# Optimization experiments

Hardware: AMD Instinct MI355X
Metric: run time of the kernel (lower is better)

## Reference

```python
import jax, jax.numpy as jnp
import numpy as np

B, SE, SD, E, H, V, O = 16, 128, 128, 512, 1024, 32000, 32000


def setup_inputs() -> dict:
    key = jax.random.key(0)
    ks = jax.random.split(key, 14)
    s = 0.02  # small init keeps tanh RNN stable
    return {
        "enc_x": jax.random.randint(ks[0], (B, SE), 0, V),
        "dec_y": jax.random.randint(ks[1], (B, SD), 0, V),
        "state0": jnp.zeros((B, H), jnp.float32),
        "emb": jax.random.normal(ks[2], (V, E), jnp.float32) * s,
        "enc_Wih": jax.random.normal(ks[3], (H, E), jnp.float32) * s,
        "enc_Whh": jax.random.normal(ks[4], (H, H), jnp.float32) * s,
        "enc_b": jax.random.normal(ks[5], (H,), jnp.float32) * s,
        "mlp1_W": jax.random.normal(ks[6], (H, H), jnp.float32) * s,
        "mlp1_b": jax.random.normal(ks[7], (H,), jnp.float32) * s,
        "dec_Wih": jax.random.normal(ks[8], (H, E + H), jnp.float32) * s,
        "dec_Whh": jax.random.normal(ks[9], (H, H), jnp.float32) * s,
        "dec_b": jax.random.normal(ks[10], (H,), jnp.float32) * s,
        "mlp2_W": jax.random.normal(ks[11], (O, H), jnp.float32) * s,
        "mlp2_b": jax.random.normal(ks[12], (O,), jnp.float32) * s,
    }


def _forward(enc_x, dec_y, state0, emb, enc_Wih, enc_Whh, enc_b,
             mlp1_W, mlp1_b, dec_Wih, dec_Whh, dec_b, mlp2_W, mlp2_b):
    # ---- encoder: vanilla tanh RNN over time ----
    enc_emb = emb[enc_x]                      # (B, SE, E)
    xs = jnp.swapaxes(enc_emb, 0, 1)          # (SE, B, E)

    def enc_step(h, x_t):
        h = jnp.tanh(x_t @ enc_Wih.T + h @ enc_Whh.T + enc_b)
        return h, h

    state, hs = jax.lax.scan(enc_step, state0, xs)
    enc_hidden = jnp.swapaxes(hs, 0, 1)       # (B, SE, H)

    # ---- decoder: per-step dot-product attention over encoder states ----
    dec_emb = emb[dec_y]                      # (B, SD, E)
    ys = jnp.swapaxes(dec_emb, 0, 1)          # (SD, B, E)

    def dec_step(h, e_t):
        q = h @ mlp1_W.T + mlp1_b                         # (B, H) query
        scores = jnp.einsum('bsh,bh->bs', enc_hidden, q)  # dot-product scores
        attn = jax.nn.softmax(scores, axis=-1)            # (B, SE)
        ctx = jnp.einsum('bs,bsh->bh', attn, enc_hidden)  # (B, H)
        x_t = jnp.concatenate([e_t, ctx], axis=-1)        # (B, E+H)
        h = jnp.tanh(x_t @ dec_Wih.T + h @ dec_Whh.T + dec_b)
        out = h @ mlp2_W.T + mlp2_b                       # (B, O)
        return h, out

    state, outs = jax.lax.scan(dec_step, state, ys)
    sent_outputs = jnp.swapaxes(outs, 0, 1)   # (B, SD, O)
    return sent_outputs, state


def reference(enc_x, dec_y, state0, emb, enc_Wih, enc_Whh, enc_b,
              mlp1_W, mlp1_b, dec_Wih, dec_Whh, dec_b, mlp2_W, mlp2_b):
    sent_outputs, state = _forward(enc_x, dec_y, state0, emb, enc_Wih, enc_Whh,
                                   enc_b, mlp1_W, mlp1_b, dec_Wih, dec_Whh,
                                   dec_b, mlp2_W, mlp2_b)
    return sent_outputs
```

## Files before the change

### kernel.cpp

```cpp
#include <hip/hip_runtime.h>
#include <hip/hip_bf16.h>

constexpr int kB  = 16;
constexpr int kSE = 128;
constexpr int kSD = 128;
constexpr int kE  = 512;
constexpr int kH  = 1024;
constexpr int kO  = 32000;

__global__ __launch_bounds__(128) void gather_rows(
    const float* __restrict__ emb, const int* __restrict__ idx,
    float* __restrict__ out)
{
    int r = blockIdx.x;
    int t = threadIdx.x;
    const float4* src = (const float4*)(emb + (size_t)idx[r] * kE);
    float4* dst = (float4*)(out + (size_t)r * kE);
    dst[t] = src[t];
}

__global__ __launch_bounds__(256) void transpose1024(
    const float* __restrict__ in, float* __restrict__ out)
{
    __shared__ float tile[32][33];
    int bx = blockIdx.x * 32, by = blockIdx.y * 32;
    int tx = threadIdx.x, ty = threadIdx.y;
    for (int i = ty; i < 32; i += 8)
        tile[i][tx] = in[(size_t)(by + i) * kH + bx + tx];
    __syncthreads();
    for (int i = ty; i < 32; i += 8)
        out[(size_t)(bx + i) * kH + by + tx] = tile[tx][i];
}

constexpr int BM = 128, BN = 128, BK = 16, LDP = 132;

__global__ __launch_bounds__(256, 2) void gemm_nt(
    const float* __restrict__ A, int lda,
    const float* __restrict__ Bmat, int ldb,
    float* __restrict__ C, int ldc,
    const float* __restrict__ bias, int K)
{
    __shared__ float As[BK][LDP];
    __shared__ float Bs[BK][LDP];

    const int bn = blockIdx.x, bm = blockIdx.y;
    const int tid = threadIdx.x;
    const int tm = tid & 15;
    const int tn = tid >> 4;

    const float* Ab = A    + (size_t)bm * BM * lda;
    const float* Bb = Bmat + (size_t)bn * BN * ldb;

    const int sr = tid >> 1;
    const int sc = (tid & 1) * 8;

    float acc[8][8];
    #pragma unroll
    for (int i = 0; i < 8; ++i)
        #pragma unroll
        for (int j = 0; j < 8; ++j) acc[i][j] = 0.f;

    for (int k0 = 0; k0 < K; k0 += BK) {
        const float4 a0 = *(const float4*)(Ab + (size_t)sr * lda + k0 + sc);
        const float4 a1 = *(const float4*)(Ab + (size_t)sr * lda + k0 + sc + 4);
        const float4 b0 = *(const float4*)(Bb + (size_t)sr * ldb + k0 + sc);
        const float4 b1 = *(const float4*)(Bb + (size_t)sr * ldb + k0 + sc + 4);
        __syncthreads();
        As[sc + 0][sr] = a0.x; As[sc + 1][sr] = a0.y;
        As[sc + 2][sr] = a0.z; As[sc + 3][sr] = a0.w;
        As[sc + 4][sr] = a1.x; As[sc + 5][sr] = a1.y;
        As[sc + 6][sr] = a1.z; As[sc + 7][sr] = a1.w;
        Bs[sc + 0][sr] = b0.x; Bs[sc + 1][sr] = b0.y;
        Bs[sc + 2][sr] = b0.z; Bs[sc + 3][sr] = b0.w;
        Bs[sc + 4][sr] = b1.x; Bs[sc + 5][sr] = b1.y;
        Bs[sc + 6][sr] = b1.z; Bs[sc + 7][sr] = b1.w;
        __syncthreads();

        #pragma unroll
        for (int k = 0; k < BK; ++k) {
            const float4 fa0 = *(const float4*)&As[k][tm * 8];
            const float4 fa1 = *(const float4*)&As[k][tm * 8 + 4];
            const float4 fb0 = *(const float4*)&Bs[k][tn * 8];
            const float4 fb1 = *(const float4*)&Bs[k][tn * 8 + 4];
            const float am[8] = {fa0.x, fa0.y, fa0.z, fa0.w,
                                 fa1.x, fa1.y, fa1.z, fa1.w};
            const float bb[8] = {fb0.x, fb0.y, fb0.z, fb0.w,
                                 fb1.x, fb1.y, fb1.z, fb1.w};
            #pragma unroll
            for (int i = 0; i < 8; ++i)
                #pragma unroll
                for (int j = 0; j < 8; ++j)
                    acc[i][j] += am[i] * bb[j];
        }
    }

    float bv[8];
    if (bias) {
        const float4 t0 = *(const float4*)&bias[bn * BN + tn * 8];
        const float4 t1 = *(const float4*)&bias[bn * BN + tn * 8 + 4];
        bv[0] = t0.x; bv[1] = t0.y; bv[2] = t0.z; bv[3] = t0.w;
        bv[4] = t1.x; bv[5] = t1.y; bv[6] = t1.z; bv[7] = t1.w;
    } else {
        #pragma unroll
        for (int j = 0; j < 8; ++j) bv[j] = 0.f;
    }
    #pragma unroll
    for (int i = 0; i < 8; ++i) {
        const size_t row = (size_t)(bm * BM + tm * 8 + i);
        float* cp = C + row * (size_t)ldc + bn * BN + tn * 8;
        float4 o0 = {acc[i][0] + bv[0], acc[i][1] + bv[1],
                     acc[i][2] + bv[2], acc[i][3] + bv[3]};
        float4 o1 = {acc[i][4] + bv[4], acc[i][5] + bv[5],
                     acc[i][6] + bv[6], acc[i][7] + bv[7]};
        *(float4*)cp = o0;
        *(float4*)(cp + 4) = o1;
    }
}

__global__ __launch_bounds__(256) void dot_bias(
    const float* __restrict__ Mrows, const float* __restrict__ v,
    float* __restrict__ out)
{
    int w = (blockIdx.x * blockDim.x + threadIdx.x) >> 6;
    int lane = threadIdx.x & 63;
    const float* row = Mrows + (size_t)w * kH;
    float s = 0.f;
    for (int k = lane; k < kH; k += 64) s += row[k] * v[k];
    #pragma unroll
    for (int off = 32; off > 0; off >>= 1) s += __shfl_xor(s, off);
    if (lane == 0) out[w] = s;
}

__global__ __launch_bounds__(64) void enc_step(
    const float* __restrict__ X, const float* __restrict__ hin,
    const float* __restrict__ Whh, float* __restrict__ hout,
    float* __restrict__ hist, int t)
{
    const int b = blockIdx.y;
    const int j = blockIdx.x * 64 + threadIdx.x;
    const float* hr = hin + b * kH;
    const float* wr = Whh + (size_t)j * kH;
    float a0 = 0, a1 = 0, a2 = 0, a3 = 0, a4 = 0, a5 = 0, a6 = 0, a7 = 0;
    #pragma unroll 4
    for (int k = 0; k < kH; k += 8) {
        const float4 h0 = *(const float4*)(hr + k);
        const float4 h1 = *(const float4*)(hr + k + 4);
        const float4 w0 = *(const float4*)(wr + k);
        const float4 w1 = *(const float4*)(wr + k + 4);
        a0 += h0.x * w0.x; a1 += h0.y * w0.y; a2 += h0.z * w0.z; a3 += h0.w * w0.w;
        a4 += h1.x * w1.x; a5 += h1.y * w1.y; a6 += h1.z * w1.z; a7 += h1.w * w1.w;
    }
    const float acc = X[((size_t)b * kSE + t) * kH + j] +
                      ((a0 + a1) + (a2 + a3)) + ((a4 + a5) + (a6 + a7));
    const float r = tanhf(acc);
    hout[b * kH + j] = r;
    hist[((size_t)b * kSE + t) * kH + j] = r;
}

__global__ __launch_bounds__(256) void attn_step(
    const float* __restrict__ Aw, const float* __restrict__ cb,
    const float* __restrict__ hin, const float* __restrict__ EH,
    float* __restrict__ ctx)
{
    __shared__ float hl[kH];
    __shared__ float sc[kSE];
    const int b = blockIdx.x;
    const int tid = threadIdx.x;
    const int lane = tid & 63;
    const int w = tid >> 6;

    for (int k = tid; k < kH; k += 256) hl[k] = hin[b * kH + k];
    __syncthreads();

    for (int s = w; s < kSE; s += 4) {
        const float* ar = Aw + ((size_t)b * kSE + s) * kH;
        float p = 0.f;
        for (int k = lane; k < kH; k += 64) p += ar[k] * hl[k];
        #pragma unroll
        for (int off = 32; off > 0; off >>= 1) p += __shfl_xor(p, off);
        if (lane == 0) sc[s] = p + cb[b * kSE + s];
    }
    __syncthreads();

    if (w == 0) {
        float v0 = sc[lane], v1 = sc[lane + 64];
        float m = fmaxf(v0, v1);
        #pragma unroll
        for (int off = 32; off > 0; off >>= 1) m = fmaxf(m, __shfl_xor(m, off));
        const float e0 = expf(v0 - m), e1 = expf(v1 - m);
        float s = e0 + e1;
        #pragma unroll
        for (int off = 32; off > 0; off >>= 1) s += __shfl_xor(s, off);
        const float inv = 1.f / s;
        sc[lane] = e0 * inv;
        sc[lane + 64] = e1 * inv;
    }
    __syncthreads();

    for (int j = tid; j < kH; j += 256) {
        float a0 = 0.f, a1 = 0.f;
        #pragma unroll 2
        for (int s = 0; s < kSE; s += 2) {
            a0 += sc[s]     * EH[((size_t)b * kSE + s)     * kH + j];
            a1 += sc[s + 1] * EH[((size_t)b * kSE + s + 1) * kH + j];
        }
        ctx[b * kH + j] = a0 + a1;
    }
}

__global__ __launch_bounds__(64) void dec_hstep(
    const float* __restrict__ X, const float* __restrict__ ctx,
    const float* __restrict__ Wih, const float* __restrict__ Whh,
    const float* __restrict__ hin, float* __restrict__ hout,
    float* __restrict__ Hs, int t)
{
    const int b = blockIdx.y;
    const int j = blockIdx.x * 64 + threadIdx.x;
    const float* cr = ctx + b * kH;
    const float* hr = hin + b * kH;
    const float* wc = Wih + (size_t)j * (kE + kH) + kE;
    const float* wh = Whh + (size_t)j * kH;
    float a0 = 0, a1 = 0, a2 = 0, a3 = 0, a4 = 0, a5 = 0, a6 = 0, a7 = 0;
    #pragma unroll 4
    for (int k = 0; k < kH; k += 4) {
        const float4 cv = *(const float4*)(cr + k);
        const float4 wv = *(const float4*)(wc + k);
        const float4 hv = *(const float4*)(hr + k);
        const float4 uv = *(const float4*)(wh + k);
        a0 += cv.x * wv.x; a1 += cv.y * wv.y; a2 += cv.z * wv.z; a3 += cv.w * wv.w;
        a4 += hv.x * uv.x; a5 += hv.y * uv.y; a6 += hv.z * uv.z; a7 += hv.w * uv.w;
    }
    const float acc = X[((size_t)b * kSD + t) * kH + j] +
                      ((a0 + a1) + (a2 + a3)) + ((a4 + a5) + (a6 + a7));
    const float r = tanhf(acc);
    hout[b * kH + j] = r;
    Hs[((size_t)b * kSD + t) * kH + j] = r;
}

extern "C" void kernel_launch(void* const* d_in, const int* in_sizes, int n_in,
                              void* d_out, int out_size, void* d_ws, size_t ws_size,
                              hipStream_t stream)
{
    const int*   enc_x   = (const int*)  d_in[0];
    const int*   dec_y   = (const int*)  d_in[1];
    const float* state0  = (const float*)d_in[2];
    const float* emb     = (const float*)d_in[3];
    const float* enc_Wih = (const float*)d_in[4];
    const float* enc_Whh = (const float*)d_in[5];
    const float* enc_b   = (const float*)d_in[6];
    const float* mlp1_W  = (const float*)d_in[7];
    const float* mlp1_b  = (const float*)d_in[8];
    const float* dec_Wih = (const float*)d_in[9];
    const float* dec_Whh = (const float*)d_in[10];
    const float* dec_b   = (const float*)d_in[11];
    const float* mlp2_W  = (const float*)d_in[12];
    const float* mlp2_b  = (const float*)d_in[13];
    float* out = (float*)d_out;

    float* ws = (float*)d_ws;
    size_t off = 0;
    const int R = kB * kSE;
    float* EncEmb = ws + off; off += (size_t)R * kE;
    float* DecEmb = ws + off; off += (size_t)R * kE;
    float* Xenc   = ws + off; off += (size_t)R * kH;
    float* Xdec   = ws + off; off += (size_t)R * kH;
    float* EH     = ws + off; off += (size_t)R * kH;
    float* Aw     = ws + off; off += (size_t)R * kH;
    float* W1T    = ws + off; off += (size_t)kH * kH;
    float* cbv    = ws + off; off += R;
    float* h0     = ws + off; off += kB * kH;
    float* h1     = ws + off; off += kB * kH;
    float* ctx    = ws + off; off += kB * kH;
    float* Hs     = ws + off; off += (size_t)R * kH;
    float* hbuf[2] = {h0, h1};

    gather_rows<<<R, 128, 0, stream>>>(emb, enc_x, EncEmb);
    gather_rows<<<R, 128, 0, stream>>>(emb, dec_y, DecEmb);

    gemm_nt<<<dim3(kH / BN, R / BM), 256, 0, stream>>>(
        EncEmb, kE, enc_Wih, kE, Xenc, kH, enc_b, kE);
    gemm_nt<<<dim3(kH / BN, R / BM), 256, 0, stream>>>(
        DecEmb, kE, dec_Wih, kE + kH, Xdec, kH, dec_b, kE);

    hipMemcpyAsync(h0, state0, (size_t)kB * kH * sizeof(float),
                   hipMemcpyDeviceToDevice, stream);

    for (int t = 0; t < kSE; ++t) {
        enc_step<<<dim3(kH / 64, kB), 64, 0, stream>>>(
            Xenc, hbuf[t & 1], enc_Whh, hbuf[(t + 1) & 1], EH, t);
    }

    transpose1024<<<dim3(32, 32), dim3(32, 8), 0, stream>>>(mlp1_W, W1T);
    gemm_nt<<<dim3(kH / BN, R / BM), 256, 0, stream>>>(
        EH, kH, W1T, kH, Aw, kH, nullptr, kH);
    dot_bias<<<R / 4, 256, 0, stream>>>(EH, mlp1_b, cbv);

    for (int t = 0; t < kSD; ++t) {
        attn_step<<<kB, 256, 0, stream>>>(Aw, cbv, hbuf[t & 1], EH, ctx);
        dec_hstep<<<dim3(kH / 64, kB), 64, 0, stream>>>(
            Xdec, ctx, dec_Wih, dec_Whh, hbuf[t & 1], hbuf[(t + 1) & 1], Hs, t);
    }

    gemm_nt<<<dim3(kO / BN, R / BM), 256, 0, stream>>>(
        Hs, kH, mlp2_W, kH, out, kO, mlp2_b, kH);
}
```

Baseline: 18.19 ms.

## Transpose recurrent weights, batch-pair recurrent steps, and use bf16 MFMA output GEMM

The recurrent weight matrices are pre-transposed so each encoder and decoder step reads weights coalesced along k. Each thread now computes two batch rows against a batch-interleaved hidden-state layout. Attention runs 1024 threads per batch with float4 score loads and writes a transposed context. The large vocabulary projection moves to a bf16 MFMA GEMM, which converts fp32 operands on the fly and adds rounding error. Workspace buffers are aliased (W1T into Hs, the transposed Whh copies into the embedding buffers), which depends on the order in which those buffers are used.

```diff
diff --git a/kernel.cpp b/kernel.cpp
--- a/kernel.cpp
+++ b/kernel.cpp
@@ -8,6 +8,9 @@
 constexpr int kH  = 1024;
 constexpr int kO  = 32000;
 
+using f32x4  = __attribute__((ext_vector_type(4))) float;
+using bf16x8 = __attribute__((ext_vector_type(8))) short;
+
 __global__ __launch_bounds__(128) void gather_rows(
     const float* __restrict__ emb, const int* __restrict__ idx,
     float* __restrict__ out)
@@ -19,17 +22,17 @@
     dst[t] = src[t];
 }
 
-__global__ __launch_bounds__(256) void transpose1024(
-    const float* __restrict__ in, float* __restrict__ out)
+__global__ __launch_bounds__(256) void transpose_k(
+    const float* __restrict__ in, int ldin, int coff, float* __restrict__ out)
 {
     __shared__ float tile[32][33];
     int bx = blockIdx.x * 32, by = blockIdx.y * 32;
     int tx = threadIdx.x, ty = threadIdx.y;
     for (int i = ty; i < 32; i += 8)
-        tile[i][tx] = in[(size_t)(by + i) * kH + bx + tx];
+        tile[i][tx] = in[(size_t)(bx + i) * ldin + coff + by + tx];
     __syncthreads();
     for (int i = ty; i < 32; i += 8)
-        out[(size_t)(bx + i) * kH + by + tx] = tile[tx][i];
+        out[(size_t)(by + i) * kH + bx + tx] = tile[tx][i];
 }
 
 constexpr int BM = 128, BN = 128, BK = 16, LDP = 132;
@@ -131,36 +134,45 @@
     if (lane == 0) out[w] = s;
 }
 
-__global__ __launch_bounds__(64) void enc_step(
-    const float* __restrict__ X, const float* __restrict__ hin,
-    const float* __restrict__ Whh, float* __restrict__ hout,
-    float* __restrict__ hist, int t)
-{
-    const int b = blockIdx.y;
-    const int j = blockIdx.x * 64 + threadIdx.x;
-    const float* hr = hin + b * kH;
-    const float* wr = Whh + (size_t)j * kH;
-    float a0 = 0, a1 = 0, a2 = 0, a3 = 0, a4 = 0, a5 = 0, a6 = 0, a7 = 0;
-    #pragma unroll 4
-    for (int k = 0; k < kH; k += 8) {
-        const float4 h0 = *(const float4*)(hr + k);
-        const float4 h1 = *(const float4*)(hr + k + 4);
-        const float4 w0 = *(const float4*)(wr + k);
-        const float4 w1 = *(const float4*)(wr + k + 4);
-        a0 += h0.x * w0.x; a1 += h0.y * w0.y; a2 += h0.z * w0.z; a3 += h0.w * w0.w;
-        a4 += h1.x * w1.x; a5 += h1.y * w1.y; a6 += h1.z * w1.z; a7 += h1.w * w1.w;
-    }
-    const float acc = X[((size_t)b * kSE + t) * kH + j] +
-                      ((a0 + a1) + (a2 + a3)) + ((a4 + a5) + (a6 + a7));
-    const float r = tanhf(acc);
-    hout[b * kH + j] = r;
-    hist[((size_t)b * kSE + t) * kH + j] = r;
-}
-
-__global__ __launch_bounds__(256) void attn_step(
-    const float* __restrict__ Aw, const float* __restrict__ cb,
-    const float* __restrict__ hin, const float* __restrict__ EH,
-    float* __restrict__ ctx)
+__global__ __launch_bounds__(1024) void init_h(
+    const float* __restrict__ s0, float* __restrict__ ht0,
+    float* __restrict__ hrow0)
+{
+    int b = blockIdx.x, j = threadIdx.x;
+    float v = s0[b * kH + j];
+    ht0[j * 16 + b] = v;
+    hrow0[b * kH + j] = v;
+}
+
+__global__ __launch_bounds__(128) void enc_step2(
+    const float* __restrict__ X, const float* __restrict__ WhhT,
+    const float* __restrict__ ht_in, float* __restrict__ ht_out,
+    float* __restrict__ hrow_out, float* __restrict__ EH, int t)
+{
+    const int j  = blockIdx.x * 128 + threadIdx.x;
+    const int b0 = blockIdx.y * 2;
+    float a0 = 0.f, a1 = 0.f;
+    #pragma unroll 8
+    for (int k = 0; k < kH; ++k) {
+        const float w = WhhT[(size_t)k * kH + j];
+        const float2 hv = *(const float2*)(ht_in + k * 16 + b0);
+        a0 += w * hv.x;
+        a1 += w * hv.y;
+    }
+    const float r0 = tanhf(X[((size_t)b0 * kSE + t) * kH + j] + a0);
+    const float r1 = tanhf(X[((size_t)(b0 + 1) * kSE + t) * kH + j] + a1);
+    ht_out[j * 16 + b0]     = r0;
+    ht_out[j * 16 + b0 + 1] = r1;
+    hrow_out[(size_t)b0 * kH + j]       = r0;
+    hrow_out[(size_t)(b0 + 1) * kH + j] = r1;
+    EH[((size_t)b0 * kSE + t) * kH + j]       = r0;
+    EH[((size_t)(b0 + 1) * kSE + t) * kH + j] = r1;
+}
+
+__global__ __launch_bounds__(1024) void attn_step2(
+    const float* __restrict__ Aw, const float* __restrict__ cbv,
+    const float* __restrict__ hrow, const float* __restrict__ EH,
+    float* __restrict__ ctx_t)
 {
     __shared__ float hl[kH];
     __shared__ float sc[kSE];
@@ -169,16 +181,24 @@
     const int lane = tid & 63;
     const int w = tid >> 6;
 
-    for (int k = tid; k < kH; k += 256) hl[k] = hin[b * kH + k];
+    hl[tid] = hrow[(size_t)b * kH + tid];
     __syncthreads();
 
-    for (int s = w; s < kSE; s += 4) {
+    #pragma unroll
+    for (int i = 0; i < 8; ++i) {
+        const int s = w * 8 + i;
         const float* ar = Aw + ((size_t)b * kSE + s) * kH;
         float p = 0.f;
-        for (int k = lane; k < kH; k += 64) p += ar[k] * hl[k];
+        #pragma unroll
+        for (int it = 0; it < 4; ++it) {
+            const int k = it * 256 + lane * 4;
+            const float4 av = *(const float4*)(ar + k);
+            const float4 hv = *(const float4*)(hl + k);
+            p += av.x * hv.x + av.y * hv.y + av.z * hv.z + av.w * hv.w;
+        }
         #pragma unroll
         for (int off = 32; off > 0; off >>= 1) p += __shfl_xor(p, off);
-        if (lane == 0) sc[s] = p + cb[b * kSE + s];
+        if (lane == 0) sc[s] = p + cbv[b * kSE + s];
     }
     __syncthreads();
 
@@ -197,44 +217,136 @@
     }
     __syncthreads();
 
-    for (int j = tid; j < kH; j += 256) {
-        float a0 = 0.f, a1 = 0.f;
-        #pragma unroll 2
-        for (int s = 0; s < kSE; s += 2) {
-            a0 += sc[s]     * EH[((size_t)b * kSE + s)     * kH + j];
-            a1 += sc[s + 1] * EH[((size_t)b * kSE + s + 1) * kH + j];
+    float acc = 0.f;
+    #pragma unroll 8
+    for (int s = 0; s < kSE; ++s)
+        acc += sc[s] * EH[((size_t)b * kSE + s) * kH + tid];
+    ctx_t[tid * 16 + b] = acc;
+}
+
+__global__ __launch_bounds__(128) void dec_step2(
+    const float* __restrict__ X, const float* __restrict__ WhhT,
+    const float* __restrict__ WcT, const float* __restrict__ ht_in,
+    const float* __restrict__ ctx_t, float* __restrict__ ht_out,
+    float* __restrict__ hrow_out, float* __restrict__ Hs, int t)
+{
+    const int j  = blockIdx.x * 128 + threadIdx.x;
+    const int b0 = blockIdx.y * 2;
+    float a0 = 0.f, a1 = 0.f;
+    #pragma unroll 4
+    for (int k = 0; k < kH; ++k) {
+        const float wh = WhhT[(size_t)k * kH + j];
+        const float wc = WcT [(size_t)k * kH + j];
+        const float2 hv = *(const float2*)(ht_in + k * 16 + b0);
+        const float2 cv = *(const float2*)(ctx_t + k * 16 + b0);
+        a0 += wh * hv.x + wc * cv.x;
+        a1 += wh * hv.y + wc * cv.y;
+    }
+    const float r0 = tanhf(X[((size_t)b0 * kSD + t) * kH + j] + a0);
+    const float r1 = tanhf(X[((size_t)(b0 + 1) * kSD + t) * kH + j] + a1);
+    ht_out[j * 16 + b0]     = r0;
+    ht_out[j * 16 + b0 + 1] = r1;
+    hrow_out[(size_t)b0 * kH + j]       = r0;
+    hrow_out[(size_t)(b0 + 1) * kH + j] = r1;
+    Hs[((size_t)b0 * kSD + t) * kH + j]       = r0;
+    Hs[((size_t)(b0 + 1) * kSD + t) * kH + j] = r1;
+}
+
+__device__ __forceinline__ unsigned pk_bf16(float x, float y) {
+    union { float f; unsigned u; } a{x}, b{y};
+    unsigned ra = (a.u + 0x7fffu + ((a.u >> 16) & 1u)) >> 16;
+    unsigned rb = (b.u + 0x7fffu + ((b.u >> 16) & 1u)) >> 16;
+    return (ra & 0xffffu) | (rb << 16);
+}
+
+constexpr int GBK = 32;
+
+__global__ __launch_bounds__(256) void gemm_bf16_nt(
+    const float* __restrict__ A, int lda,
+    const float* __restrict__ Bmat, int ldb,
+    float* __restrict__ C, int ldc,
+    const float* __restrict__ bias, int K)
+{
+    __shared__ short As[128 * GBK];
+    __shared__ short Bs[128 * GBK];
+
+    const int tid  = threadIdx.x;
+    const int wave = tid >> 6, lane = tid & 63;
+    const int wr = wave >> 1, wc = wave & 1;
+    const int bm = blockIdx.y, bn = blockIdx.x;
+
+    const float* Ab = A    + (size_t)bm * 128 * lda;
+    const float* Bb = Bmat + (size_t)bn * 128 * ldb;
+
+    const int srow = tid >> 1;
+    const int sk   = (tid & 1) * 16;
+
+    const int frow = lane & 15;
+    const int kgrp = lane >> 4;
+
+    f32x4 acc[4][4];
+    #pragma unroll
+    for (int m = 0; m < 4; ++m)
+        #pragma unroll
+        for (int n = 0; n < 4; ++n) acc[m][n] = (f32x4)(0.f);
+
+    for (int k0 = 0; k0 < K; k0 += GBK) {
+        const float* ap = Ab + (size_t)srow * lda + k0 + sk;
+        const float* bp = Bb + (size_t)srow * ldb + k0 + sk;
+        const float4 a0 = *(const float4*)(ap);
+        const float4 a1 = *(const float4*)(ap + 4);
+        const float4 a2 = *(const float4*)(ap + 8);
+        const float4 a3 = *(const float4*)(ap + 12);
+        const float4 b0 = *(const float4*)(bp);
+        const float4 b1 = *(const float4*)(bp + 4);
+        const float4 b2 = *(const float4*)(bp + 8);
+        const float4 b3 = *(const float4*)(bp + 12);
+        __syncthreads();
+        int4 wA0 = {(int)pk_bf16(a0.x, a0.y), (int)pk_bf16(a0.z, a0.w),
+                    (int)pk_bf16(a1.x, a1.y), (int)pk_bf16(a1.z, a1.w)};
+        int4 wA1 = {(int)pk_bf16(a2.x, a2.y), (int)pk_bf16(a2.z, a2.w),
+                    (int)pk_bf16(a3.x, a3.y), (int)pk_bf16(a3.z, a3.w)};
+        int4 wB0 = {(int)pk_bf16(b0.x, b0.y), (int)pk_bf16(b0.z, b0.w),
+                    (int)pk_bf16(b1.x, b1.y), (int)pk_bf16(b1.z, b1.w)};
+        int4 wB1 = {(int)pk_bf16(b2.x, b2.y), (int)pk_bf16(b2.z, b2.w),
+                    (int)pk_bf16(b3.x, b3.y), (int)pk_bf16(b3.z, b3.w)};
+        *(int4*)&As[srow * GBK + sk]     = wA0;
+        *(int4*)&As[srow * GBK + sk + 8] = wA1;
+        *(int4*)&Bs[srow * GBK + sk]     = wB0;
+        *(int4*)&Bs[srow * GBK + sk + 8] = wB1;
+        __syncthreads();
+
+        bf16x8 af[4], bf[4];
+        #pragma unroll
+        for (int m = 0; m < 4; ++m)
+            af[m] = *(const bf16x8*)&As[(wr * 64 + m * 16 + frow) * GBK + kgrp * 8];
+        #pragma unroll
+        for (int n = 0; n < 4; ++n)
+            bf[n] = *(const bf16x8*)&Bs[(wc * 64 + n * 16 + frow) * GBK + kgrp * 8];
+        #pragma unroll
+        for (int m = 0; m < 4; ++m)
+            #pragma unroll
+            for (int n = 0; n < 4; ++n)
+                acc[m][n] = __builtin_amdgcn_mfma_f32_16x16x32_bf16(
+                    af[m], bf[n], acc[m][n], 0, 0, 0);
+    }
+
+    float bv[4];
+    #pragma unroll
+    for (int n = 0; n < 4; ++n)
+        bv[n] = bias ? bias[bn * 128 + wc * 64 + n * 16 + frow] : 0.f;
+    #pragma unroll
+    for (int m = 0; m < 4; ++m) {
+        #pragma unroll
+        for (int n = 0; n < 4; ++n) {
+            const int col = bn * 128 + wc * 64 + n * 16 + frow;
+            #pragma unroll
+            for (int r = 0; r < 4; ++r) {
+                const int row = bm * 128 + wr * 64 + m * 16 + kgrp * 4 + r;
+                C[(size_t)row * ldc + col] = acc[m][n][r] + bv[n];
+            }
         }
-        ctx[b * kH + j] = a0 + a1;
-    }
-}
-
-__global__ __launch_bounds__(64) void dec_hstep(
-    const float* __restrict__ X, const float* __restrict__ ctx,
-    const float* __restrict__ Wih, const float* __restrict__ Whh,
-    const float* __restrict__ hin, float* __restrict__ hout,
-    float* __restrict__ Hs, int t)
-{
-    const int b = blockIdx.y;
-    const int j = blockIdx.x * 64 + threadIdx.x;
-    const float* cr = ctx + b * kH;
-    const float* hr = hin + b * kH;
-    const float* wc = Wih + (size_t)j * (kE + kH) + kE;
-    const float* wh = Whh + (size_t)j * kH;
-    float a0 = 0, a1 = 0, a2 = 0, a3 = 0, a4 = 0, a5 = 0, a6 = 0, a7 = 0;
-    #pragma unroll 4
-    for (int k = 0; k < kH; k += 4) {
-        const float4 cv = *(const float4*)(cr + k);
-        const float4 wv = *(const float4*)(wc + k);
-        const float4 hv = *(const float4*)(hr + k);
-        const float4 uv = *(const float4*)(wh + k);
-        a0 += cv.x * wv.x; a1 += cv.y * wv.y; a2 += cv.z * wv.z; a3 += cv.w * wv.w;
-        a4 += hv.x * uv.x; a5 += hv.y * uv.y; a6 += hv.z * uv.z; a7 += hv.w * uv.w;
-    }
-    const float acc = X[((size_t)b * kSD + t) * kH + j] +
-                      ((a0 + a1) + (a2 + a3)) + ((a4 + a5) + (a6 + a7));
-    const float r = tanhf(acc);
-    hout[b * kH + j] = r;
-    Hs[((size_t)b * kSD + t) * kH + j] = r;
+    }
 }
 
 extern "C" void kernel_launch(void* const* d_in, const int* in_sizes, int n_in,
@@ -260,19 +372,25 @@
     float* ws = (float*)d_ws;
     size_t off = 0;
     const int R = kB * kSE;
-    float* EncEmb = ws + off; off += (size_t)R * kE;
-    float* DecEmb = ws + off; off += (size_t)R * kE;
     float* Xenc   = ws + off; off += (size_t)R * kH;
     float* Xdec   = ws + off; off += (size_t)R * kH;
     float* EH     = ws + off; off += (size_t)R * kH;
     float* Aw     = ws + off; off += (size_t)R * kH;
-    float* W1T    = ws + off; off += (size_t)kH * kH;
+    float* Hs     = ws + off; off += (size_t)R * kH;
+    float* W1T    = Hs;
+    float* WcT    = ws + off; off += (size_t)kH * kH;
+    float* EncEmb = ws + off; off += (size_t)R * kE;
+    float* WhhTe  = EncEmb;
+    float* DecEmb = ws + off; off += (size_t)R * kE;
+    float* WhhTd  = DecEmb;
     float* cbv    = ws + off; off += R;
-    float* h0     = ws + off; off += kB * kH;
-    float* h1     = ws + off; off += kB * kH;
-    float* ctx    = ws + off; off += kB * kH;
-    float* Hs     = ws + off; off += (size_t)R * kH;
-    float* hbuf[2] = {h0, h1};
+    float* ht0    = ws + off; off += kB * kH;
+    float* ht1    = ws + off; off += kB * kH;
+    float* hrow0  = ws + off; off += kB * kH;
+    float* hrow1  = ws + off; off += kB * kH;
+    float* ctxT   = ws + off; off += kB * kH;
+    float* htb[2]   = {ht0, ht1};
+    float* hrowb[2] = {hrow0, hrow1};
 
     gather_rows<<<R, 128, 0, stream>>>(emb, enc_x, EncEmb);
     gather_rows<<<R, 128, 0, stream>>>(emb, dec_y, DecEmb);
@@ -282,25 +400,30 @@
     gemm_nt<<<dim3(kH / BN, R / BM), 256, 0, stream>>>(
         DecEmb, kE, dec_Wih, kE + kH, Xdec, kH, dec_b, kE);
 
-    hipMemcpyAsync(h0, state0, (size_t)kB * kH * sizeof(float),
-                   hipMemcpyDeviceToDevice, stream);
+    transpose_k<<<dim3(32, 32), dim3(32, 8), 0, stream>>>(enc_Whh, kH, 0, WhhTe);
+    transpose_k<<<dim3(32, 32), dim3(32, 8), 0, stream>>>(dec_Whh, kH, 0, WhhTd);
+    transpose_k<<<dim3(32, 32), dim3(32, 8), 0, stream>>>(dec_Wih, kE + kH, kE, WcT);
+    transpose_k<<<dim3(32, 32), dim3(32, 8), 0, stream>>>(mlp1_W, kH, 0, W1T);
+
+    init_h<<<kB, kH, 0, stream>>>(state0, ht0, hrow0);
 
     for (int t = 0; t < kSE; ++t) {
-        enc_step<<<dim3(kH / 64, kB), 64, 0, stream>>>(
-            Xenc, hbuf[t & 1], enc_Whh, hbuf[(t + 1) & 1], EH, t);
-    }
-
-    transpose1024<<<dim3(32, 32), dim3(32, 8), 0, stream>>>(mlp1_W, W1T);
+        enc_step2<<<dim3(8, 8), 128, 0, stream>>>(
+            Xenc, WhhTe, htb[t & 1], htb[(t + 1) & 1], hrowb[(t + 1) & 1], EH, t);
+    }
+
     gemm_nt<<<dim3(kH / BN, R / BM), 256, 0, stream>>>(
         EH, kH, W1T, kH, Aw, kH, nullptr, kH);
     dot_bias<<<R / 4, 256, 0, stream>>>(EH, mlp1_b, cbv);
 
     for (int t = 0; t < kSD; ++t) {
-        attn_step<<<kB, 256, 0, stream>>>(Aw, cbv, hbuf[t & 1], EH, ctx);
-        dec_hstep<<<dim3(kH / 64, kB), 64, 0, stream>>>(
-            Xdec, ctx, dec_Wih, dec_Whh, hbuf[t & 1], hbuf[(t + 1) & 1], Hs, t);
-    }
-
-    gemm_nt<<<dim3(kO / BN, R / BM), 256, 0, stream>>>(
+        attn_step2<<<kB, 1024, 0, stream>>>(
+            Aw, cbv, hrowb[t & 1], EH, ctxT);
+        dec_step2<<<dim3(8, 8), 128, 0, stream>>>(
+            Xdec, WhhTd, WcT, htb[t & 1], ctxT,
+            htb[(t + 1) & 1], hrowb[(t + 1) & 1], Hs, t);
+    }
+
+    gemm_bf16_nt<<<dim3(kO / 128, R / 128), 256, 0, stream>>>(
         Hs, kH, mlp2_W, kH, out, kO, mlp2_b, kH);
 }
```

Result: slower. 27.65 ms (+52.1%).
